# Kernel tuning notes

Measured on AMD Instinct MI355X. Metric: run time of the kernel, lower is better.

## Reference

```python
import jax, jax.numpy as jnp
import numpy as np

TEMP = 0.5   # temperature from __init__
EPS = 1e-8   # torch.nn.CosineSimilarity eps


def setup_inputs() -> dict:
    key = jax.random.key(0)
    N, D = 8192, 256
    x = jax.random.normal(key, (N, D), dtype=jnp.float32)
    # pairs: each label appears exactly twice, as required for the
    # sim[~mask].reshape(N, -1) in the original to be well-formed
    y = jnp.arange(N, dtype=jnp.int32) // 2
    return {"x": x, "y": y}


def reference(x, y):
    # cosine similarity matrix: normalize once, then one NxD @ DxN matmul
    # (equivalent to CosineSimilarity(x.unsqueeze(1), x.unsqueeze(0)) without
    #  the NxNxD intermediate)
    norm = jnp.maximum(jnp.linalg.norm(x, axis=1, keepdims=True), EPS)
    xn = x / norm
    sim = (xn @ xn.T) / TEMP                     # [N, N]

    # Original: positives = equal-label entries (row-major order, includes the
    # diagonal), logits = [positives | negatives] which is just a per-row
    # permutation of sim; labels = 0 -> CE target is the FIRST equal-label
    # column of each row. logsumexp is over the full row (all N entries).
    eq = y[:, None] == y[None, :]                # [N, N] bool
    first_pos = jnp.argmax(eq, axis=1)           # first column j with y_j == y_i
    target = jnp.take_along_axis(sim, first_pos[:, None], axis=1)[:, 0]  # [N]

    lse = jax.nn.logsumexp(sim, axis=1)          # [N]
    N = x.shape[0]
    loss = jnp.sum(lse - target) / N             # CrossEntropyLoss(sum) / N
    return loss
```

## Files before the change

### kernel.cpp

```cpp
#include <hip/hip_runtime.h>
#include <hip/hip_bf16.h>

#define D 256
#define INV_TEMP 2.0f

typedef __attribute__((ext_vector_type(8))) short short8;
typedef __attribute__((ext_vector_type(4))) float floatx4;

__device__ __forceinline__ unsigned short f2bf(float f) {
    union { float f; unsigned u; } a; a.f = f;
    unsigned r = (a.u + 0x7fffu + ((a.u >> 16) & 1u)) >> 16;
    return (unsigned short)r;
}

__device__ __forceinline__ void gload_lds16(const unsigned short* g,
                                            unsigned short* l) {
    __builtin_amdgcn_global_load_lds(
        (const __attribute__((address_space(1))) unsigned int*)g,
        (__attribute__((address_space(3))) unsigned int*)l, 16, 0, 0);
}

__global__ void nt_prep_kernel(const float* __restrict__ x,
                               unsigned short* __restrict__ xnb,
                               float* __restrict__ pair_dot) {
    int p    = blockIdx.x * 4 + (threadIdx.x >> 6);
    int lane = threadIdx.x & 63;
    const float4* a4 = (const float4*)(x + (size_t)(2 * p) * D);
    const float4* b4 = (const float4*)(x + (size_t)(2 * p + 1) * D);
    float4 a = a4[lane], b = b4[lane];
    float saa = a.x * a.x + a.y * a.y + a.z * a.z + a.w * a.w;
    float sbb = b.x * b.x + b.y * b.y + b.z * b.z + b.w * b.w;
    float sab = a.x * b.x + a.y * b.y + a.z * b.z + a.w * b.w;
    #pragma unroll
    for (int off = 32; off; off >>= 1) {
        saa += __shfl_xor(saa, off);
        sbb += __shfl_xor(sbb, off);
        sab += __shfl_xor(sab, off);
    }
    float inva = 1.0f / fmaxf(sqrtf(saa), 1e-8f);
    float invb = 1.0f / fmaxf(sqrtf(sbb), 1e-8f);
    ushort4 oa, ob;
    oa.x = f2bf(a.x * inva); oa.y = f2bf(a.y * inva);
    oa.z = f2bf(a.z * inva); oa.w = f2bf(a.w * inva);
    ob.x = f2bf(b.x * invb); ob.y = f2bf(b.y * invb);
    ob.z = f2bf(b.z * invb); ob.w = f2bf(b.w * invb);
    ((ushort4*)(xnb + (size_t)(2 * p) * D))[lane] = oa;
    ((ushort4*)(xnb + (size_t)(2 * p + 1) * D))[lane] = ob;
    if (lane == 0)
        pair_dot[p] = sab * inva * invb * INV_TEMP;
}

__global__ __launch_bounds__(256, 1)
void nt_simexp_kernel(const unsigned short* __restrict__ xnb,
                      float* __restrict__ contrib) {
    __shared__ __align__(16) unsigned short Bs[128 * 256];
    __shared__ __align__(16) unsigned short As[2][128 * 128];

    const int p = blockIdx.x >> 3, q = blockIdx.x & 7;
    const int n1 = 64 - p;

    const int tid  = threadIdx.x;
    const int wave = tid >> 6, lane = tid & 63;
    const int wm   = wave & 1, wn = wave >> 1;
    const int quad = lane >> 4, c = lane & 15;

    auto tile_of = [&](int i, int& bi, int& bj) {
        if (i < n1) { bi = p + i;      bj = p; }
        else        { bi = 63 - p + (i - n1); bj = 63 - p; }
    };

    auto load_B = [&](int bj) {
        const unsigned short* src = xnb + (size_t)(bj * 128) * D;
        int rsub = lane >> 5, pp = lane & 31;
        #pragma unroll
        for (int t = 0; t < 16; ++t) {
            int wl = wave * 16 + t;
            int rr = wl * 2 + rsub;
            int j  = (pp & ~7) | ((pp ^ rr) & 7);
            gload_lds16(src + (size_t)rr * D + j * 8, Bs + wl * 512 + lane * 8);
        }
    };
    auto load_A = [&](int bi, int kb, unsigned short* Ab) {
        const unsigned short* src = xnb + (size_t)(bi * 128) * D + kb * 128;
        int rsub = lane >> 4, pp = lane & 15;
        #pragma unroll
        for (int t = 0; t < 8; ++t) {
            int wl = wave * 8 + t;
            int rr = wl * 4 + rsub;
            int jl = (pp & 8) | ((pp ^ rr) & 7);
            gload_lds16(src + (size_t)rr * D + jl * 8, Ab + wl * 512 + lane * 8);
        }
    };

    floatx4 acc[4][4];
    auto compute = [&](const unsigned short* Ab, int kb) {
        #pragma unroll
        for (int kl = 0; kl < 4; ++kl) {
            int jl = kl * 4 + quad;
            int pA = (jl & 8) | ((jl ^ c) & 7);
            int jg = kb * 16 + jl;
            int pB = (jg & ~7) | ((jg ^ c) & 7);
            short8 af[4], bf[4];
            #pragma unroll
            for (int mt = 0; mt < 4; ++mt)
                af[mt] = *(const short8*)(Ab + (wm * 64 + mt * 16 + c) * 128 + pA * 8);
            #pragma unroll
            for (int nt = 0; nt < 4; ++nt)
                bf[nt] = *(const short8*)(Bs + (wn * 64 + nt * 16 + c) * 256 + pB * 8);
            #pragma unroll
            for (int mt = 0; mt < 4; ++mt)
                #pragma unroll
                for (int nt = 0; nt < 4; ++nt)
                    acc[mt][nt] = __builtin_amdgcn_mfma_f32_16x16x32_bf16(
                        af[mt], bf[nt], acc[mt][nt], 0, 0, 0);
        }
    };

    const int m = (q == 0) ? 9 : 8;
    int bi, bj;
    tile_of(q, bi, bj);
    load_B(bj);
    load_A(bi, 0, As[0]);
    __syncthreads();

    for (int j = 0; j < m; ++j) {
        tile_of(q + 8 * j, bi, bj);
        bool have_next = (j + 1 < m);
        int nbi = 0, nbj = 0;
        if (have_next) tile_of(q + 8 * (j + 1), nbi, nbj);
        bool same = have_next && (nbj == bj);

        #pragma unroll
        for (int mt = 0; mt < 4; ++mt)
            #pragma unroll
            for (int nt = 0; nt < 4; ++nt)
                acc[mt][nt] = (floatx4){0.f, 0.f, 0.f, 0.f};

        load_A(bi, 1, As[1]);
        compute(As[0], 0);
        __syncthreads();
        if (same) load_A(nbi, 0, As[0]);
        compute(As[1], 1);

        #pragma unroll
        for (int mt = 0; mt < 4; ++mt)
            #pragma unroll
            for (int nt = 0; nt < 4; ++nt)
                #pragma unroll
                for (int r = 0; r < 4; ++r)
                    acc[mt][nt][r] = __expf(acc[mt][nt][r] * INV_TEMP);

        #pragma unroll
        for (int mt = 0; mt < 4; ++mt) {
            float ps[4] = {0.f, 0.f, 0.f, 0.f};
            #pragma unroll
            for (int nt = 0; nt < 4; ++nt)
                #pragma unroll
                for (int r = 0; r < 4; ++r)
                    ps[r] += acc[mt][nt][r];
            #pragma unroll
            for (int off = 1; off < 16; off <<= 1)
                #pragma unroll
                for (int r = 0; r < 4; ++r)
                    ps[r] += __shfl_xor(ps[r], off);
            if (c == 0) {
                float4 v = {ps[0], ps[1], ps[2], ps[3]};
                *(float4*)(contrib + (((size_t)bi * 64 + bj) * 2 + wn) * 128 +
                           wm * 64 + mt * 16 + quad * 4) = v;
            }
        }
        if (bi != bj) {
            #pragma unroll
            for (int nt = 0; nt < 4; ++nt) {
                float cs = 0.f;
                #pragma unroll
                for (int mt = 0; mt < 4; ++mt)
                    #pragma unroll
                    for (int r = 0; r < 4; ++r)
                        cs += acc[mt][nt][r];
                cs += __shfl_xor(cs, 16);
                cs += __shfl_xor(cs, 32);
                if (quad == 0)
                    contrib[(((size_t)bj * 64 + bi) * 2 + wm) * 128 +
                            wn * 64 + nt * 16 + c] = cs;
            }
        }
        __syncthreads();
        if (have_next && !same) {
            load_B(nbj);
            load_A(nbi, 0, As[0]);
            __syncthreads();
        }
    }
}

__global__ void nt_reduce_kernel(const float* __restrict__ contrib,
                                 const float* __restrict__ pair_dot,
                                 float* __restrict__ blockPart) {
    __shared__ float sm[256];
    int b  = blockIdx.x;
    int rl = threadIdx.x & 127, h = threadIdx.x >> 7;
    float s = 0.f;
    const float* base = contrib + (((size_t)b * 64) * 2 + h) * 128 + rl;
    #pragma unroll
    for (int j = 0; j < 64; ++j) s += base[(size_t)j * 256];
    sm[threadIdx.x] = s;
    __syncthreads();
    float v = 0.f;
    if (h == 0) v = logf(sm[rl] + sm[128 + rl]);
    else if (rl < 64) v = -pair_dot[b * 64 + rl];
    __syncthreads();
    sm[threadIdx.x] = v;
    __syncthreads();
    for (int st = 128; st; st >>= 1) {
        if ((int)threadIdx.x < st) sm[threadIdx.x] += sm[threadIdx.x + st];
        __syncthreads();
    }
    if (threadIdx.x == 0) blockPart[b] = sm[0];
}

__global__ void nt_final_kernel(const float* __restrict__ blockPart,
                                float* __restrict__ out, int N) {
    int lane = threadIdx.x & 63;
    float s = blockPart[lane];
    #pragma unroll
    for (int off = 32; off; off >>= 1) s += __shfl_xor(s, off);
    if (lane == 0) out[0] = (s - (float)N) / (float)N;
}

extern "C" void kernel_launch(void* const* d_in, const int* in_sizes, int n_in,
                              void* d_out, int out_size, void* d_ws, size_t ws_size,
                              hipStream_t stream) {
    const float* x = (const float*)d_in[0];
    int N = in_sizes[0] / D;

    char* ws = (char*)d_ws;
    unsigned short* xnb = (unsigned short*)ws;
    float* pair_dot  = (float*)(ws + (size_t)N * D * 2);
    float* contrib   = pair_dot + N / 2;
    float* blockPart = contrib + (size_t)64 * 64 * 2 * 128;

    nt_prep_kernel<<<N / 8, 256, 0, stream>>>(x, xnb, pair_dot);
    nt_simexp_kernel<<<256, 256, 0, stream>>>(xnb, contrib);
    nt_reduce_kernel<<<N / 128, 256, 0, stream>>>(contrib, pair_dot, blockPart);
    nt_final_kernel<<<1, 64, 0, stream>>>(blockPart, (float*)d_out, N);
}
```

Before: 107.5 us.

## Process two row-tiles per block with 8 waves and 4-phase K pipeline

The sim-exp kernel now uses 512 threads (8 waves) and handles a 256x128 unit made of two adjacent 128-row A tiles sharing one B tile, which halves the B-tile loads per A tile. The K loop is split into four 64-wide phases with double-buffered A staging, and the next unit's B/A loads are issued before the exp/reduction epilogue so they overlap it. Odd tile counts are handled with a validity flag on the second half. Launch bounds ask for 2 blocks per CU, which caps registers per thread and adds more barriers per unit.

```diff
diff --git a/kernel.cpp b/kernel.cpp
--- a/kernel.cpp
+++ b/kernel.cpp
@@ -50,60 +50,63 @@
         pair_dot[p] = sab * inva * invb * INV_TEMP;
 }
 
-__global__ __launch_bounds__(256, 1)
+__global__ __launch_bounds__(512, 2)
 void nt_simexp_kernel(const unsigned short* __restrict__ xnb,
                       float* __restrict__ contrib) {
     __shared__ __align__(16) unsigned short Bs[128 * 256];
-    __shared__ __align__(16) unsigned short As[2][128 * 128];
-
-    const int p = blockIdx.x >> 3, q = blockIdx.x & 7;
-    const int n1 = 64 - p;
+    __shared__ __align__(16) unsigned short As[2][256 * 64];
+
+    const int p  = blockIdx.x >> 3, q = blockIdx.x & 7;
+    const int s1 = 63 - p;
+    const int c0 = 64 - p, c1 = p + 1;
+    const int u0 = (c0 + 1) >> 1;
+    const int uT = u0 + ((c1 + 1) >> 1);
 
     const int tid  = threadIdx.x;
     const int wave = tid >> 6, lane = tid & 63;
-    const int wm   = wave & 1, wn = wave >> 1;
+    const int wm   = wave & 3, wn = wave >> 2;
     const int quad = lane >> 4, c = lane & 15;
 
-    auto tile_of = [&](int i, int& bi, int& bj) {
-        if (i < n1) { bi = p + i;      bj = p; }
-        else        { bi = 63 - p + (i - n1); bj = 63 - p; }
+    auto unit_of = [&](int i, int& bi0, int& bj, bool& v2) {
+        if (i < u0) { bi0 = p + 2 * i; bj = p; v2 = (2 * i + 1 < c0); }
+        else { int jj = i - u0; bi0 = s1 + 2 * jj; bj = s1; v2 = (2 * jj + 1 < c1); }
     };
 
     auto load_B = [&](int bj) {
         const unsigned short* src = xnb + (size_t)(bj * 128) * D;
-        int rsub = lane >> 5, pp = lane & 31;
-        #pragma unroll
-        for (int t = 0; t < 16; ++t) {
-            int wl = wave * 16 + t;
-            int rr = wl * 2 + rsub;
+        int rs = lane >> 5, pp = lane & 31;
+        #pragma unroll
+        for (int t = 0; t < 8; ++t) {
+            int wl = wave * 8 + t;
+            int rr = wl * 2 + rs;
             int j  = (pp & ~7) | ((pp ^ rr) & 7);
             gload_lds16(src + (size_t)rr * D + j * 8, Bs + wl * 512 + lane * 8);
         }
     };
-    auto load_A = [&](int bi, int kb, unsigned short* Ab) {
-        const unsigned short* src = xnb + (size_t)(bi * 128) * D + kb * 128;
-        int rsub = lane >> 4, pp = lane & 15;
-        #pragma unroll
-        for (int t = 0; t < 8; ++t) {
-            int wl = wave * 8 + t;
-            int rr = wl * 4 + rsub;
-            int jl = (pp & 8) | ((pp ^ rr) & 7);
-            gload_lds16(src + (size_t)rr * D + jl * 8, Ab + wl * 512 + lane * 8);
+    auto load_A = [&](int bi0, int ph, unsigned short* Ab) {
+        const unsigned short* src = xnb + ((size_t)bi0 * 128) * D + ph * 64;
+        int rs = lane >> 3, pp = lane & 7;
+        #pragma unroll
+        for (int t = 0; t < 4; ++t) {
+            int wl = wave * 4 + t;
+            int rr = wl * 8 + rs;
+            int j  = pp ^ (rr & 7);
+            gload_lds16(src + (size_t)rr * D + j * 8, Ab + wl * 512 + lane * 8);
         }
     };
 
     floatx4 acc[4][4];
-    auto compute = [&](const unsigned short* Ab, int kb) {
-        #pragma unroll
-        for (int kl = 0; kl < 4; ++kl) {
+    auto compute = [&](const unsigned short* Ab, int ph) {
+        #pragma unroll
+        for (int kl = 0; kl < 2; ++kl) {
             int jl = kl * 4 + quad;
-            int pA = (jl & 8) | ((jl ^ c) & 7);
-            int jg = kb * 16 + jl;
+            int pA = jl ^ (c & 7);
+            int jg = ph * 8 + jl;
             int pB = (jg & ~7) | ((jg ^ c) & 7);
             short8 af[4], bf[4];
             #pragma unroll
             for (int mt = 0; mt < 4; ++mt)
-                af[mt] = *(const short8*)(Ab + (wm * 64 + mt * 16 + c) * 128 + pA * 8);
+                af[mt] = *(const short8*)(Ab + (wm * 64 + mt * 16 + c) * 64 + pA * 8);
             #pragma unroll
             for (int nt = 0; nt < 4; ++nt)
                 bf[nt] = *(const short8*)(Bs + (wn * 64 + nt * 16 + c) * 256 + pB * 8);
@@ -116,19 +119,17 @@
         }
     };
 
-    const int m = (q == 0) ? 9 : 8;
-    int bi, bj;
-    tile_of(q, bi, bj);
+    int bi0, bj; bool v2;
+    unit_of(q, bi0, bj, v2);
     load_B(bj);
-    load_A(bi, 0, As[0]);
-    __syncthreads();
-
-    for (int j = 0; j < m; ++j) {
-        tile_of(q + 8 * j, bi, bj);
-        bool have_next = (j + 1 < m);
-        int nbi = 0, nbj = 0;
-        if (have_next) tile_of(q + 8 * (j + 1), nbi, nbj);
-        bool same = have_next && (nbj == bj);
+    load_A(bi0, 0, As[0]);
+    __syncthreads();
+
+    for (int i = q; i < uT; i += 8) {
+        unit_of(i, bi0, bj, v2);
+        int nbi0 = 0, nbj = -1; bool nv2 = false;
+        if (i + 8 < uT) unit_of(i + 8, nbi0, nbj, nv2);
+        const bool same = (nbj == bj);
 
         #pragma unroll
         for (int mt = 0; mt < 4; ++mt)
@@ -136,11 +137,18 @@
             for (int nt = 0; nt < 4; ++nt)
                 acc[mt][nt] = (floatx4){0.f, 0.f, 0.f, 0.f};
 
-        load_A(bi, 1, As[1]);
-        compute(As[0], 0);
-        __syncthreads();
-        if (same) load_A(nbi, 0, As[0]);
-        compute(As[1], 1);
+        #pragma unroll
+        for (int ph = 0; ph < 4; ++ph) {
+            if (ph < 3) load_A(bi0, ph + 1, As[(ph + 1) & 1]);
+            else if (same) load_A(nbi0, 0, As[0]);
+            compute(As[ph & 1], ph);
+            __syncthreads();
+        }
+
+        if (nbj >= 0 && !same) {
+            load_B(nbj);
+            load_A(nbi0, 0, As[0]);
+        }
 
         #pragma unroll
         for (int mt = 0; mt < 4; ++mt)
@@ -150,6 +158,9 @@
                 for (int r = 0; r < 4; ++r)
                     acc[mt][nt][r] = __expf(acc[mt][nt][r] * INV_TEMP);
 
+        const int  bi_x = bi0 + (wm >> 1);
+        const bool rv   = ((wm >> 1) == 0) || v2;
+
         #pragma unroll
         for (int mt = 0; mt < 4; ++mt) {
             float ps[4] = {0.f, 0.f, 0.f, 0.f};
@@ -163,13 +174,13 @@
                 #pragma unroll
                 for (int r = 0; r < 4; ++r)
                     ps[r] += __shfl_xor(ps[r], off);
-            if (c == 0) {
+            if (c == 0 && rv) {
                 float4 v = {ps[0], ps[1], ps[2], ps[3]};
-                *(float4*)(contrib + (((size_t)bi * 64 + bj) * 2 + wn) * 128 +
-                           wm * 64 + mt * 16 + quad * 4) = v;
+                *(float4*)(contrib + (((size_t)bi_x * 64 + bj) * 2 + wn) * 128 +
+                           (wm & 1) * 64 + mt * 16 + quad * 4) = v;
             }
         }
-        if (bi != bj) {
+        if (bi_x != bj && rv) {
             #pragma unroll
             for (int nt = 0; nt < 4; ++nt) {
                 float cs = 0.f;
@@ -181,16 +192,11 @@
                 cs += __shfl_xor(cs, 16);
                 cs += __shfl_xor(cs, 32);
                 if (quad == 0)
-                    contrib[(((size_t)bj * 64 + bi) * 2 + wm) * 128 +
+                    contrib[(((size_t)bj * 64 + bi_x) * 2 + (wm & 1)) * 128 +
                             wn * 64 + nt * 16 + c] = cs;
             }
         }
-        __syncthreads();
-        if (have_next && !same) {
-            load_B(nbj);
-            load_A(nbi, 0, As[0]);
-            __syncthreads();
-        }
+        if (nbj >= 0 && !same) __syncthreads();
     }
 }
 
@@ -241,7 +247,7 @@
     float* blockPart = contrib + (size_t)64 * 64 * 2 * 128;
 
     nt_prep_kernel<<<N / 8, 256, 0, stream>>>(x, xnb, pair_dot);
-    nt_simexp_kernel<<<256, 256, 0, stream>>>(xnb, contrib);
+    nt_simexp_kernel<<<256, 512, 0, stream>>>(xnb, contrib);
     nt_reduce_kernel<<<N / 128, 256, 0, stream>>>(contrib, pair_dot, blockPart);
     nt_final_kernel<<<1, 64, 0, stream>>>(blockPart, (float*)d_out, N);
 }
```

Result: faster. 102.4 us (-4.7%).

## Shrink A-tile LDS staging to allow two blocks per CU and double grid

Applied to the files above, without the earlier changes.

The A operand is now staged in 32-wide K slices, double-buffered over eight phases, so LDS use drops from about 128KB to about 80KB per block. Launch bounds go to two blocks per CU and the grid doubles to 512 blocks, with each of 16 blocks per strip walking tiles in a rotated order. The next strip's B and A loads are issued before the exp and reduction epilogue so they overlap it. The cost is more barriers per tile (one per phase) and a register budget halved by the occupancy hint, which may cause spills with 64 accumulator floats per thread.

```diff
diff --git a/kernel.cpp b/kernel.cpp
--- a/kernel.cpp
+++ b/kernel.cpp
@@ -50,85 +50,79 @@
         pair_dot[p] = sab * inva * invb * INV_TEMP;
 }
 
-__global__ __launch_bounds__(256, 1)
+__global__ __launch_bounds__(256, 2)
 void nt_simexp_kernel(const unsigned short* __restrict__ xnb,
                       float* __restrict__ contrib) {
     __shared__ __align__(16) unsigned short Bs[128 * 256];
-    __shared__ __align__(16) unsigned short As[2][128 * 128];
-
-    const int p = blockIdx.x >> 3, q = blockIdx.x & 7;
-    const int n1 = 64 - p;
+    __shared__ __align__(16) unsigned short As[2][128 * 32];
+
+    const int p  = blockIdx.x >> 4, q = blockIdx.x & 15;
+    const int s1 = 63 - p;
+    const int c0 = 64 - p;
+    const int q0 = (p + q) & 15;
 
     const int tid  = threadIdx.x;
     const int wave = tid >> 6, lane = tid & 63;
     const int wm   = wave & 1, wn = wave >> 1;
     const int quad = lane >> 4, c = lane & 15;
 
-    auto tile_of = [&](int i, int& bi, int& bj) {
-        if (i < n1) { bi = p + i;      bj = p; }
-        else        { bi = 63 - p + (i - n1); bj = 63 - p; }
-    };
+    auto strip_of = [&](int i) { return (i < c0) ? p : s1; };
+    auto bi_of    = [&](int i) { return (i < c0) ? (p + i) : (s1 + i - c0); };
 
     auto load_B = [&](int bj) {
         const unsigned short* src = xnb + (size_t)(bj * 128) * D;
-        int rsub = lane >> 5, pp = lane & 31;
+        int rs = lane >> 5, pp = lane & 31;
         #pragma unroll
         for (int t = 0; t < 16; ++t) {
             int wl = wave * 16 + t;
-            int rr = wl * 2 + rsub;
+            int rr = wl * 2 + rs;
             int j  = (pp & ~7) | ((pp ^ rr) & 7);
             gload_lds16(src + (size_t)rr * D + j * 8, Bs + wl * 512 + lane * 8);
         }
     };
-    auto load_A = [&](int bi, int kb, unsigned short* Ab) {
-        const unsigned short* src = xnb + (size_t)(bi * 128) * D + kb * 128;
-        int rsub = lane >> 4, pp = lane & 15;
-        #pragma unroll
-        for (int t = 0; t < 8; ++t) {
-            int wl = wave * 8 + t;
-            int rr = wl * 4 + rsub;
-            int jl = (pp & 8) | ((pp ^ rr) & 7);
-            gload_lds16(src + (size_t)rr * D + jl * 8, Ab + wl * 512 + lane * 8);
+    auto load_A = [&](int bi, int ph, unsigned short* Ab) {
+        const unsigned short* src = xnb + (size_t)(bi * 128) * D + ph * 32;
+        int rl = lane >> 2, pq = lane & 3;
+        #pragma unroll
+        for (int t = 0; t < 2; ++t) {
+            int wl = wave * 2 + t;
+            int rr = wl * 16 + rl;
+            int j  = pq ^ ((rr >> 1) & 3);
+            gload_lds16(src + (size_t)rr * D + j * 8, Ab + wl * 512 + lane * 8);
         }
     };
 
     floatx4 acc[4][4];
-    auto compute = [&](const unsigned short* Ab, int kb) {
-        #pragma unroll
-        for (int kl = 0; kl < 4; ++kl) {
-            int jl = kl * 4 + quad;
-            int pA = (jl & 8) | ((jl ^ c) & 7);
-            int jg = kb * 16 + jl;
-            int pB = (jg & ~7) | ((jg ^ c) & 7);
-            short8 af[4], bf[4];
-            #pragma unroll
-            for (int mt = 0; mt < 4; ++mt)
-                af[mt] = *(const short8*)(Ab + (wm * 64 + mt * 16 + c) * 128 + pA * 8);
-            #pragma unroll
-            for (int nt = 0; nt < 4; ++nt)
-                bf[nt] = *(const short8*)(Bs + (wn * 64 + nt * 16 + c) * 256 + pB * 8);
-            #pragma unroll
-            for (int mt = 0; mt < 4; ++mt)
-                #pragma unroll
-                for (int nt = 0; nt < 4; ++nt)
-                    acc[mt][nt] = __builtin_amdgcn_mfma_f32_16x16x32_bf16(
-                        af[mt], bf[nt], acc[mt][nt], 0, 0, 0);
-        }
+    auto compute = [&](const unsigned short* Ab, int ph) {
+        const int pA = quad ^ ((c >> 1) & 3);
+        const int jg = ph * 4 + quad;
+        const int pB = (jg & ~7) | ((jg ^ c) & 7);
+        short8 af[4], bf[4];
+        #pragma unroll
+        for (int mt = 0; mt < 4; ++mt)
+            af[mt] = *(const short8*)(Ab + (wm * 64 + mt * 16 + c) * 32 + pA * 8);
+        #pragma unroll
+        for (int nt = 0; nt < 4; ++nt)
+            bf[nt] = *(const short8*)(Bs + (wn * 64 + nt * 16 + c) * 256 + pB * 8);
+        #pragma unroll
+        for (int mt = 0; mt < 4; ++mt)
+            #pragma unroll
+            for (int nt = 0; nt < 4; ++nt)
+                acc[mt][nt] = __builtin_amdgcn_mfma_f32_16x16x32_bf16(
+                    af[mt], bf[nt], acc[mt][nt], 0, 0, 0);
     };
 
-    const int m = (q == 0) ? 9 : 8;
-    int bi, bj;
-    tile_of(q, bi, bj);
+    int bj = strip_of(q0);
     load_B(bj);
-    load_A(bi, 0, As[0]);
-    __syncthreads();
-
-    for (int j = 0; j < m; ++j) {
-        tile_of(q + 8 * j, bi, bj);
-        bool have_next = (j + 1 < m);
-        int nbi = 0, nbj = 0;
-        if (have_next) tile_of(q + 8 * (j + 1), nbi, nbj);
-        bool same = have_next && (nbj == bj);
+    load_A(bi_of(q0), 0, As[0]);
+    __syncthreads();
+
+    for (int i = q0; i < 65; i += 16) {
+        const int bi = bi_of(i);
+        const int ni = i + 16;
+        const bool have_next = (ni < 65);
+        const int nbj = have_next ? strip_of(ni) : -1;
+        const bool same = have_next && (nbj == bj);
 
         #pragma unroll
         for (int mt = 0; mt < 4; ++mt)
@@ -136,11 +130,18 @@
             for (int nt = 0; nt < 4; ++nt)
                 acc[mt][nt] = (floatx4){0.f, 0.f, 0.f, 0.f};
 
-        load_A(bi, 1, As[1]);
-        compute(As[0], 0);
-        __syncthreads();
-        if (same) load_A(nbi, 0, As[0]);
-        compute(As[1], 1);
+        #pragma unroll
+        for (int ph = 0; ph < 8; ++ph) {
+            if (ph < 7) load_A(bi, ph + 1, As[(ph + 1) & 1]);
+            else if (same) load_A(bi_of(ni), 0, As[0]);
+            compute(As[ph & 1], ph);
+            __syncthreads();
+        }
+
+        if (have_next && !same) {
+            load_B(nbj);
+            load_A(bi_of(ni), 0, As[0]);
+        }
 
         #pragma unroll
         for (int mt = 0; mt < 4; ++mt)
@@ -185,11 +186,9 @@
                             wn * 64 + nt * 16 + c] = cs;
             }
         }
-        __syncthreads();
         if (have_next && !same) {
-            load_B(nbj);
-            load_A(nbi, 0, As[0]);
             __syncthreads();
+            bj = nbj;
         }
     }
 }
@@ -241,7 +240,7 @@
     float* blockPart = contrib + (size_t)64 * 64 * 2 * 128;
 
     nt_prep_kernel<<<N / 8, 256, 0, stream>>>(x, xnb, pair_dot);
-    nt_simexp_kernel<<<256, 256, 0, stream>>>(xnb, contrib);
+    nt_simexp_kernel<<<512, 256, 0, stream>>>(xnb, contrib);
     nt_reduce_kernel<<<N / 128, 256, 0, stream>>>(contrib, pair_dot, blockPart);
     nt_final_kernel<<<1, 64, 0, stream>>>(blockPart, (float*)d_out, N);
 }
```

Measured after the change: 101.1 us. 1.06x faster.
